# Performance work log

Hardware: AMD Instinct MI355X
Metric: run time of the kernel (lower is better)

## Reference

```python
import jax, jax.numpy as jnp
import numpy as np

B, S, D, E, K = 4, 4096, 2048, 64, 2
LN_EPS = 1e-5
TEMP_EPS = 1e-6
Z_LOSS_COEF = 0.001
LB_COEF = 0.1


def setup_inputs() -> dict:
    key = jax.random.key(0)
    k1, k2 = jax.random.split(key)
    x = jax.random.normal(k1, (B, S, D), dtype=jnp.float32)
    # kaiming_normal fan_in (std = 1/sqrt(D)) scaled by 0.01, as in __init__
    W = jax.random.normal(k2, (E, D), dtype=jnp.float32) * jnp.float32(0.01 / np.sqrt(D))
    gamma = jnp.ones((E,), jnp.float32)   # LayerNorm weight
    beta = jnp.zeros((E,), jnp.float32)   # LayerNorm bias
    temperature = jnp.full((1,), 0.5, jnp.float32)
    return {"x": x, "W": W, "gamma": gamma, "beta": beta, "temperature": temperature}


def reference(x, W, gamma, beta, temperature):
    b, s, d = x.shape
    xf = x.reshape(-1, d)                                  # [N, D]
    logits = xf @ W.T                                      # [N, E]
    # LayerNorm over expert dim (biased variance, eps=1e-5, matches torch)
    mu = logits.mean(axis=-1, keepdims=True)
    var = jnp.mean(jnp.square(logits - mu), axis=-1, keepdims=True)
    logits = (logits - mu) * jax.lax.rsqrt(var + LN_EPS) * gamma + beta
    # temperature-scaled softmax
    routing_weights = jax.nn.softmax(logits / (temperature + TEMP_EPS), axis=-1)  # [N, E]
    # top-k + scatter into dense dispatch mask
    top_w, top_idx = jax.lax.top_k(routing_weights, K)     # [N, K]
    n = routing_weights.shape[0]
    dispatch = jnp.zeros_like(routing_weights).at[jnp.arange(n)[:, None], top_idx].set(top_w)
    dispatch = dispatch.reshape(b, s, E)                   # [B, S, E]
    # aux losses
    expert_load = dispatch.mean(axis=1)                    # [B, E]
    load_balance_loss = jnp.std(expert_load, ddof=1) / expert_load.mean() * 10.0
    router_z_loss = jnp.mean(jnp.square(logits))
    total_loss = ZLC * router_z_loss + LB_COEF * load_balance_loss if False else (
        Z_LOSS_COEF * router_z_loss + LB_COEF * load_balance_loss)
    return jax.lax.stop_gradient(routing_weights), dispatch, total_loss
```

## Files before the change

kernel.cpp:

```cpp
#include <hip/hip_runtime.h>
#include <hip/hip_bf16.h>
#include <float.h>
#include <math.h>

#define B_DIM 4
#define S_DIM 4096
#define D_DIM 2048
#define E_DIM 64
#define N_TOK 16384
#define SPLITK 4
#define KSLICE (D_DIM / SPLITK)
#define MSTEP (KSLICE / 32)
#define TPB 128
#define NMAIN ((N_TOK / TPB) * SPLITK)
#define EPB 16
#define NEPI (N_TOK / EPB)
#define GAP_THRESH 1e-3f

#define WS_WLO_B   262144
#define WS_HEAD_B  524288
#define WS_PART_B  540672
#define WS_NEED    (WS_PART_B + (size_t)SPLITK * N_TOK * E_DIM * 4)
#define HEAD_ZSLOT 0
#define HEAD_LOADP 64

typedef __bf16 bf16x8_t __attribute__((ext_vector_type(8)));
typedef float f32x4_t __attribute__((ext_vector_type(4)));
union U8 { bf16x8_t v; unsigned short u[8]; };

__device__ __forceinline__ void split2(float f, unsigned short& h, unsigned short& l) {
    unsigned int u = __float_as_uint(f);
    h = (unsigned short)(u >> 16);
    float hf = __uint_as_float(u & 0xFFFF0000u);
    l = (unsigned short)(__float_as_uint(f - hf) >> 16);
}

__global__ __launch_bounds__(256) void wconv(const float* __restrict__ W,
                                             unsigned short* __restrict__ whi,
                                             unsigned short* __restrict__ wlo) {
    const int t = blockIdx.x * 256 + threadIdx.x;
    float4 v = *(const float4*)(W + (size_t)t * 4);
    ushort4 h, l;
    split2(v.x, h.x, l.x); split2(v.y, h.y, l.y);
    split2(v.z, h.z, l.z); split2(v.w, h.w, l.w);
    *(ushort4*)(whi + (size_t)t * 4) = h;
    *(ushort4*)(wlo + (size_t)t * 4) = l;
}

template<bool ATOMIC>
__global__ __launch_bounds__(256, 2) void router_main(
    const float* __restrict__ x,
    const unsigned short* __restrict__ whi, const unsigned short* __restrict__ wlo,
    float* __restrict__ part)
{
    const int tid = threadIdx.x;
    const int lane = tid & 63, wv = tid >> 6;
    const int l15 = lane & 15, quad = lane >> 4;
    const int slice = blockIdx.x & (SPLITK - 1);
    const int grp = blockIdx.x >> 2;
    const int tokBase = grp * TPB + wv * 32;
    const int k0 = slice * KSLICE;

    const float* xb[2];
    xb[0] = x + (size_t)(tokBase + l15) * D_DIM + k0 + quad * 8;
    xb[1] = x + (size_t)(tokBase + 16 + l15) * D_DIM + k0 + quad * 8;

    f32x4_t acc[2][4];
    #pragma unroll
    for (int m = 0; m < 2; ++m)
        #pragma unroll
        for (int t = 0; t < 4; ++t) acc[m][t] = (f32x4_t){0.f, 0.f, 0.f, 0.f};

    float4 xq[2][2], xn[2][2];
    #pragma unroll
    for (int m = 0; m < 2; ++m) {
        xq[m][0] = *(const float4*)(xb[m]);
        xq[m][1] = *(const float4*)(xb[m] + 4);
    }

    #pragma unroll 4
    for (int s = 0; s < MSTEP; ++s) {
        if (s + 1 < MSTEP) {
            #pragma unroll
            for (int m = 0; m < 2; ++m) {
                const float* p = xb[m] + (s + 1) * 32;
                xn[m][0] = *(const float4*)(p);
                xn[m][1] = *(const float4*)(p + 4);
            }
        }
        const int kk = k0 + s * 32 + quad * 8;
        bf16x8_t bh[4], bl[4];
        #pragma unroll
        for (int t = 0; t < 4; ++t) {
            const size_t off = (size_t)(t * 16 + l15) * D_DIM + kk;
            bh[t] = *(const bf16x8_t*)(whi + off);
            bl[t] = *(const bf16x8_t*)(wlo + off);
        }
        #pragma unroll
        for (int m = 0; m < 2; ++m) {
            float tf[8] = {xq[m][0].x, xq[m][0].y, xq[m][0].z, xq[m][0].w,
                           xq[m][1].x, xq[m][1].y, xq[m][1].z, xq[m][1].w};
            U8 ah, al;
            #pragma unroll
            for (int k = 0; k < 8; ++k) split2(tf[k], ah.u[k], al.u[k]);
            #pragma unroll
            for (int t = 0; t < 4; ++t) {
                acc[m][t] = __builtin_amdgcn_mfma_f32_16x16x32_bf16(ah.v, bh[t], acc[m][t], 0, 0, 0);
                acc[m][t] = __builtin_amdgcn_mfma_f32_16x16x32_bf16(ah.v, bl[t], acc[m][t], 0, 0, 0);
                acc[m][t] = __builtin_amdgcn_mfma_f32_16x16x32_bf16(al.v, bh[t], acc[m][t], 0, 0, 0);
            }
        }
        if (s + 1 < MSTEP) {
            #pragma unroll
            for (int m = 0; m < 2; ++m) { xq[m][0] = xn[m][0]; xq[m][1] = xn[m][1]; }
        }
    }

    #pragma unroll
    for (int m = 0; m < 2; ++m)
        #pragma unroll
        for (int t = 0; t < 4; ++t)
            #pragma unroll
            for (int r = 0; r < 4; ++r) {
                const int token = tokBase + m * 16 + quad * 4 + r;
                const int e = t * 16 + l15;
                if (ATOMIC) atomicAdd(&part[(size_t)token * E_DIM + e], acc[m][t][r]);
                else part[((size_t)slice * N_TOK + token) * E_DIM + e] = acc[m][t][r];
            }
}

__device__ __forceinline__ void wave_argmax(float y, float& mv, int& mi) {
    float v = y; int ix = threadIdx.x & 63;
    #pragma unroll
    for (int d = 32; d; d >>= 1) {
        float ov = __shfl_xor(v, d); int oi = __shfl_xor(ix, d);
        if (ov > v || (ov == v && oi < ix)) { v = ov; ix = oi; }
    }
    mv = v; mi = ix;
}

template<bool ATOMIC>
__global__ __launch_bounds__(1024) void router_epi(
    const float* __restrict__ part, const float* __restrict__ x,
    const float* __restrict__ W, const float* __restrict__ gamma,
    const float* __restrict__ beta, const float* __restrict__ temperature,
    float* __restrict__ out_rw, float* __restrict__ out_dp,
    float* __restrict__ zslot, float* __restrict__ loadp)
{
    __shared__ float loadsum[E_DIM];
    __shared__ float zred[EPB];
    const int tid = threadIdx.x;
    const int lane = tid & 63, wv = tid >> 6;
    const int tok = blockIdx.x * EPB + wv;
    if (tid < E_DIM) loadsum[tid] = 0.f;
    __syncthreads();

    float p;
    if (ATOMIC) p = part[(size_t)tok * E_DIM + lane];
    else {
        p = 0.f;
        #pragma unroll
        for (int s = 0; s < SPLITK; ++s) p += part[((size_t)s * N_TOK + tok) * E_DIM + lane];
    }
    float s1 = p, s2 = p * p;
    #pragma unroll
    for (int d = 32; d; d >>= 1) { s1 += __shfl_xor(s1, d); s2 += __shfl_xor(s2, d); }
    const float mu = s1 * (1.f / 64.f);
    const float var = s2 * (1.f / 64.f) - mu * mu;
    const float rs = rsqrtf(var + 1e-5f);
    const float y = (p - mu) * rs * gamma[lane] + beta[lane];

    float zl = y * y;
    #pragma unroll
    for (int d = 32; d; d >>= 1) zl += __shfl_xor(zl, d);
    if (lane == 0) zred[wv] = zl;

    float m0, m1, m2; int i0, i1, i2;
    wave_argmax(y, m0, i0);
    wave_argmax((lane == i0) ? -FLT_MAX : y, m1, i1);
    wave_argmax((lane == i0 || lane == i1) ? -FLT_MAX : y, m2, i2);
    int sa = i0, sb = i1;

    if (m1 - m2 < GAP_THRESH) {
        const float* xr = x + (size_t)tok * D_DIM;
        const int c[3] = {i0, i1, i2};
        double L[3];
        #pragma unroll
        for (int j = 0; j < 3; ++j) {
            const float* wr = W + (size_t)c[j] * D_DIM;
            double a = 0.0;
            for (int i = lane; i < D_DIM; i += 64) a += (double)xr[i] * (double)wr[i];
            #pragma unroll
            for (int d = 32; d; d >>= 1) a += __shfl_xor(a, d);
            L[j] = a;
        }
        double yy[3];
        #pragma unroll
        for (int j = 0; j < 3; ++j)
            yy[j] = (L[j] - (double)mu) * (double)rs * (double)gamma[c[j]] + (double)beta[c[j]];
        bool g01 = (yy[0] > yy[1]) || (yy[0] == yy[1] && c[0] < c[1]);
        bool g02 = (yy[0] > yy[2]) || (yy[0] == yy[2] && c[0] < c[2]);
        bool g12 = (yy[1] > yy[2]) || (yy[1] == yy[2] && c[1] < c[2]);
        if (!g01 && !g02)     { sa = c[1]; sb = c[2]; }
        else if (g01 && !g12) { sa = c[0]; sb = c[2]; }
        else                  { sa = c[0]; sb = c[1]; }
    }

    const float it = 1.f / (temperature[0] + 1e-6f);
    float ev = __expf((y - m0) * it);
    float es = ev;
    #pragma unroll
    for (int d = 32; d; d >>= 1) es += __shfl_xor(es, d);
    const float prob = ev / es;

    out_rw[(size_t)tok * E_DIM + lane] = prob;
    const bool sel = (lane == sa || lane == sb);
    out_dp[(size_t)tok * E_DIM + lane] = sel ? prob : 0.f;
    if (sel) atomicAdd(&loadsum[lane], prob);
    __syncthreads();

    if (tid == 0) {
        float z = 0.f;
        #pragma unroll
        for (int i = 0; i < EPB; ++i) z += zred[i];
        atomicAdd(&zslot[blockIdx.x & 63], z);
    }
    const int b = (blockIdx.x * EPB) >> 12;
    if (tid < E_DIM) atomicAdd(&loadp[(blockIdx.x & 7) * 256 + b * E_DIM + tid], loadsum[tid]);
}

__global__ void router_fin(const float* __restrict__ head, float* __restrict__ out_loss) {
    __shared__ float sv[B_DIM * E_DIM];
    const int tid = threadIdx.x;
    float s = 0.f;
    #pragma unroll
    for (int pl = 0; pl < 8; ++pl) s += head[HEAD_LOADP + pl * 256 + tid];
    sv[tid] = s * (1.f / S_DIM);
    __syncthreads();
    if (tid == 0) {
        float t = 0.f;
        for (int i = 0; i < B_DIM * E_DIM; ++i) t += sv[i];
        const float mean = t * (1.f / (B_DIM * E_DIM));
        float ss = 0.f;
        for (int i = 0; i < B_DIM * E_DIM; ++i) { float d = sv[i] - mean; ss += d * d; }
        const float sd = sqrtf(ss * (1.f / (B_DIM * E_DIM - 1)));
        float z = 0.f;
        for (int i = 0; i < 64; ++i) z += head[HEAD_ZSLOT + i];
        out_loss[0] = 0.001f * (z * (1.f / ((float)N_TOK * E_DIM))) + 0.1f * (sd / mean) * 10.f;
    }
}

extern "C" void kernel_launch(void* const* d_in, const int* in_sizes, int n_in,
                              void* d_out, int out_size, void* d_ws, size_t ws_size,
                              hipStream_t stream) {
    const float* x     = (const float*)d_in[0];
    const float* W     = (const float*)d_in[1];
    const float* gamma = (const float*)d_in[2];
    const float* beta  = (const float*)d_in[3];
    const float* temp  = (const float*)d_in[4];
    float* out  = (float*)d_out;
    float* rw   = out;
    float* dp   = out + (size_t)N_TOK * E_DIM;
    float* loss = out + 2 * (size_t)N_TOK * E_DIM;

    unsigned short* whi = (unsigned short*)d_ws;
    unsigned short* wlo = (unsigned short*)((char*)d_ws + WS_WLO_B);
    float* head = (float*)((char*)d_ws + WS_HEAD_B);
    float* partbuf = (float*)((char*)d_ws + WS_PART_B);
    const bool store_path = (ws_size >= WS_NEED);

    hipMemsetAsync((char*)d_ws + WS_HEAD_B, 0, 16384, stream);
    wconv<<<dim3(128), dim3(256), 0, stream>>>(W, whi, wlo);
    if (store_path) {
        router_main<false><<<dim3(NMAIN), dim3(256), 0, stream>>>(x, whi, wlo, partbuf);
        router_epi<false><<<dim3(NEPI), dim3(1024), 0, stream>>>(
            partbuf, x, W, gamma, beta, temp, rw, dp,
            head + HEAD_ZSLOT, head + HEAD_LOADP);
    } else {
        hipMemsetAsync(rw, 0, (size_t)N_TOK * E_DIM * 4, stream);
        router_main<true><<<dim3(NMAIN), dim3(256), 0, stream>>>(x, whi, wlo, rw);
        router_epi<true><<<dim3(NEPI), dim3(1024), 0, stream>>>(
            rw, x, W, gamma, beta, temp, rw, dp,
            head + HEAD_ZSLOT, head + HEAD_LOADP);
    }
    router_fin<<<dim3(1), dim3(256), 0, stream>>>(head, loss);
}
```

Before: 270.5 us.

## Use single bf16 MFMA with LDS-staged weights and widen exact top-k fallback

Replaces the three-pass split-bf16 GEMM with a single bf16 MFMA pass using round-to-nearest conversion. Each block now stages its W slice as bf16 in LDS, which removes the separate weight-conversion kernel. To absorb the larger logit error, the gap threshold for the fp64 recheck is raised and the candidate set grows from three to four experts. The epilogue drops its LDS reductions in favour of direct per-lane global atomics, so more tokens may take the slow fp64 path and contention on the atomics goes up.

```diff
diff --git a/kernel.cpp b/kernel.cpp
--- a/kernel.cpp
+++ b/kernel.cpp
@@ -10,123 +10,88 @@
 #define N_TOK 16384
 #define SPLITK 4
 #define KSLICE (D_DIM / SPLITK)
-#define MSTEP (KSLICE / 32)
-#define TPB 128
-#define NMAIN ((N_TOK / TPB) * SPLITK)
-#define EPB 16
-#define NEPI (N_TOK / EPB)
-#define GAP_THRESH 1e-3f
-
-#define WS_WLO_B   262144
-#define WS_HEAD_B  524288
-#define WS_PART_B  540672
-#define WS_NEED    (WS_PART_B + (size_t)SPLITK * N_TOK * E_DIM * 4)
+#define STEPS (KSLICE / 32)
+#define TPB_MAIN 256
+#define NMAIN ((N_TOK / TPB_MAIN) * SPLITK)
+#define NEPI (N_TOK / 4)
+#define PITCH 520
+#define GAP_THRESH 0.02f
+
 #define HEAD_ZSLOT 0
 #define HEAD_LOADP 64
+#define WS_PART_B  16384
+#define WS_NEED    (WS_PART_B + (size_t)SPLITK * N_TOK * E_DIM * 4)
 
 typedef __bf16 bf16x8_t __attribute__((ext_vector_type(8)));
 typedef float f32x4_t __attribute__((ext_vector_type(4)));
 union U8 { bf16x8_t v; unsigned short u[8]; };
 
-__device__ __forceinline__ void split2(float f, unsigned short& h, unsigned short& l) {
+__device__ __forceinline__ unsigned short f2bf(float f) {
     unsigned int u = __float_as_uint(f);
-    h = (unsigned short)(u >> 16);
-    float hf = __uint_as_float(u & 0xFFFF0000u);
-    l = (unsigned short)(__float_as_uint(f - hf) >> 16);
-}
-
-__global__ __launch_bounds__(256) void wconv(const float* __restrict__ W,
-                                             unsigned short* __restrict__ whi,
-                                             unsigned short* __restrict__ wlo) {
-    const int t = blockIdx.x * 256 + threadIdx.x;
-    float4 v = *(const float4*)(W + (size_t)t * 4);
-    ushort4 h, l;
-    split2(v.x, h.x, l.x); split2(v.y, h.y, l.y);
-    split2(v.z, h.z, l.z); split2(v.w, h.w, l.w);
-    *(ushort4*)(whi + (size_t)t * 4) = h;
-    *(ushort4*)(wlo + (size_t)t * 4) = l;
+    u += 0x7FFFu + ((u >> 16) & 1u);
+    return (unsigned short)(u >> 16);
 }
 
 template<bool ATOMIC>
-__global__ __launch_bounds__(256, 2) void router_main(
-    const float* __restrict__ x,
-    const unsigned short* __restrict__ whi, const unsigned short* __restrict__ wlo,
+__global__ __launch_bounds__(1024, 4) void router_main(
+    const float* __restrict__ x, const float* __restrict__ W,
     float* __restrict__ part)
 {
+    __shared__ unsigned short wlds[E_DIM][PITCH];
     const int tid = threadIdx.x;
+    const int slice = blockIdx.x & (SPLITK - 1);
+    const int grp = blockIdx.x >> 2;
+
+    {
+        const int row = tid >> 4, seg = tid & 15;
+        const float* wp = W + (size_t)row * D_DIM + slice * KSLICE + seg * 32;
+        #pragma unroll
+        for (int j = 0; j < 8; ++j) {
+            float4 v = *(const float4*)(wp + j * 4);
+            ushort4 h = {f2bf(v.x), f2bf(v.y), f2bf(v.z), f2bf(v.w)};
+            *(ushort4*)&wlds[row][seg * 32 + j * 4] = h;
+        }
+    }
+    __syncthreads();
+
     const int lane = tid & 63, wv = tid >> 6;
     const int l15 = lane & 15, quad = lane >> 4;
-    const int slice = blockIdx.x & (SPLITK - 1);
-    const int grp = blockIdx.x >> 2;
-    const int tokBase = grp * TPB + wv * 32;
-    const int k0 = slice * KSLICE;
-
-    const float* xb[2];
-    xb[0] = x + (size_t)(tokBase + l15) * D_DIM + k0 + quad * 8;
-    xb[1] = x + (size_t)(tokBase + 16 + l15) * D_DIM + k0 + quad * 8;
-
-    f32x4_t acc[2][4];
-    #pragma unroll
-    for (int m = 0; m < 2; ++m)
-        #pragma unroll
-        for (int t = 0; t < 4; ++t) acc[m][t] = (f32x4_t){0.f, 0.f, 0.f, 0.f};
-
-    float4 xq[2][2], xn[2][2];
-    #pragma unroll
-    for (int m = 0; m < 2; ++m) {
-        xq[m][0] = *(const float4*)(xb[m]);
-        xq[m][1] = *(const float4*)(xb[m] + 4);
-    }
-
+    const int token0 = grp * TPB_MAIN + wv * 16;
+    const float* xp = x + (size_t)(token0 + l15) * D_DIM + slice * KSLICE + quad * 8;
+
+    f32x4_t acc[4];
+    #pragma unroll
+    for (int t = 0; t < 4; ++t) acc[t] = (f32x4_t){0.f, 0.f, 0.f, 0.f};
+
+    float4 xq0 = *(const float4*)xp;
+    float4 xq1 = *(const float4*)(xp + 4);
     #pragma unroll 4
-    for (int s = 0; s < MSTEP; ++s) {
-        if (s + 1 < MSTEP) {
-            #pragma unroll
-            for (int m = 0; m < 2; ++m) {
-                const float* p = xb[m] + (s + 1) * 32;
-                xn[m][0] = *(const float4*)(p);
-                xn[m][1] = *(const float4*)(p + 4);
-            }
-        }
-        const int kk = k0 + s * 32 + quad * 8;
-        bf16x8_t bh[4], bl[4];
+    for (int s = 0; s < STEPS; ++s) {
+        float4 xn0, xn1;
+        if (s + 1 < STEPS) {
+            xn0 = *(const float4*)(xp + (s + 1) * 32);
+            xn1 = *(const float4*)(xp + (s + 1) * 32 + 4);
+        }
+        U8 a;
+        a.u[0] = f2bf(xq0.x); a.u[1] = f2bf(xq0.y); a.u[2] = f2bf(xq0.z); a.u[3] = f2bf(xq0.w);
+        a.u[4] = f2bf(xq1.x); a.u[5] = f2bf(xq1.y); a.u[6] = f2bf(xq1.z); a.u[7] = f2bf(xq1.w);
         #pragma unroll
         for (int t = 0; t < 4; ++t) {
-            const size_t off = (size_t)(t * 16 + l15) * D_DIM + kk;
-            bh[t] = *(const bf16x8_t*)(whi + off);
-            bl[t] = *(const bf16x8_t*)(wlo + off);
-        }
-        #pragma unroll
-        for (int m = 0; m < 2; ++m) {
-            float tf[8] = {xq[m][0].x, xq[m][0].y, xq[m][0].z, xq[m][0].w,
-                           xq[m][1].x, xq[m][1].y, xq[m][1].z, xq[m][1].w};
-            U8 ah, al;
-            #pragma unroll
-            for (int k = 0; k < 8; ++k) split2(tf[k], ah.u[k], al.u[k]);
-            #pragma unroll
-            for (int t = 0; t < 4; ++t) {
-                acc[m][t] = __builtin_amdgcn_mfma_f32_16x16x32_bf16(ah.v, bh[t], acc[m][t], 0, 0, 0);
-                acc[m][t] = __builtin_amdgcn_mfma_f32_16x16x32_bf16(ah.v, bl[t], acc[m][t], 0, 0, 0);
-                acc[m][t] = __builtin_amdgcn_mfma_f32_16x16x32_bf16(al.v, bh[t], acc[m][t], 0, 0, 0);
-            }
-        }
-        if (s + 1 < MSTEP) {
-            #pragma unroll
-            for (int m = 0; m < 2; ++m) { xq[m][0] = xn[m][0]; xq[m][1] = xn[m][1]; }
-        }
-    }
-
-    #pragma unroll
-    for (int m = 0; m < 2; ++m)
-        #pragma unroll
-        for (int t = 0; t < 4; ++t)
-            #pragma unroll
-            for (int r = 0; r < 4; ++r) {
-                const int token = tokBase + m * 16 + quad * 4 + r;
-                const int e = t * 16 + l15;
-                if (ATOMIC) atomicAdd(&part[(size_t)token * E_DIM + e], acc[m][t][r]);
-                else part[((size_t)slice * N_TOK + token) * E_DIM + e] = acc[m][t][r];
-            }
+            bf16x8_t b = *(const bf16x8_t*)&wlds[t * 16 + l15][s * 32 + quad * 8];
+            acc[t] = __builtin_amdgcn_mfma_f32_16x16x32_bf16(a.v, b, acc[t], 0, 0, 0);
+        }
+        if (s + 1 < STEPS) { xq0 = xn0; xq1 = xn1; }
+    }
+
+    #pragma unroll
+    for (int t = 0; t < 4; ++t)
+        #pragma unroll
+        for (int r = 0; r < 4; ++r) {
+            const int token = token0 + quad * 4 + r;
+            const int e = t * 16 + l15;
+            if (ATOMIC) atomicAdd(&part[(size_t)token * E_DIM + e], acc[t][r]);
+            else part[((size_t)slice * N_TOK + token) * E_DIM + e] = acc[t][r];
+        }
 }
 
 __device__ __forceinline__ void wave_argmax(float y, float& mv, int& mi) {
@@ -140,20 +105,16 @@
 }
 
 template<bool ATOMIC>
-__global__ __launch_bounds__(1024) void router_epi(
+__global__ __launch_bounds__(256, 4) void router_epi(
     const float* __restrict__ part, const float* __restrict__ x,
     const float* __restrict__ W, const float* __restrict__ gamma,
     const float* __restrict__ beta, const float* __restrict__ temperature,
     float* __restrict__ out_rw, float* __restrict__ out_dp,
     float* __restrict__ zslot, float* __restrict__ loadp)
 {
-    __shared__ float loadsum[E_DIM];
-    __shared__ float zred[EPB];
     const int tid = threadIdx.x;
     const int lane = tid & 63, wv = tid >> 6;
-    const int tok = blockIdx.x * EPB + wv;
-    if (tid < E_DIM) loadsum[tid] = 0.f;
-    __syncthreads();
+    const int tok = blockIdx.x * 4 + wv;
 
     float p;
     if (ATOMIC) p = part[(size_t)tok * E_DIM + lane];
@@ -173,37 +134,36 @@
     float zl = y * y;
     #pragma unroll
     for (int d = 32; d; d >>= 1) zl += __shfl_xor(zl, d);
-    if (lane == 0) zred[wv] = zl;
-
-    float m0, m1, m2; int i0, i1, i2;
+
+    float m0, m1, m2, m3; int i0, i1, i2, i3;
     wave_argmax(y, m0, i0);
     wave_argmax((lane == i0) ? -FLT_MAX : y, m1, i1);
     wave_argmax((lane == i0 || lane == i1) ? -FLT_MAX : y, m2, i2);
+    wave_argmax((lane == i0 || lane == i1 || lane == i2) ? -FLT_MAX : y, m3, i3);
     int sa = i0, sb = i1;
 
     if (m1 - m2 < GAP_THRESH) {
         const float* xr = x + (size_t)tok * D_DIM;
-        const int c[3] = {i0, i1, i2};
-        double L[3];
-        #pragma unroll
-        for (int j = 0; j < 3; ++j) {
-            const float* wr = W + (size_t)c[j] * D_DIM;
+        const int cc[4] = {i0, i1, i2, i3};
+        double yy[4];
+        #pragma unroll
+        for (int j = 0; j < 4; ++j) {
+            const float* wr = W + (size_t)cc[j] * D_DIM;
             double a = 0.0;
             for (int i = lane; i < D_DIM; i += 64) a += (double)xr[i] * (double)wr[i];
             #pragma unroll
             for (int d = 32; d; d >>= 1) a += __shfl_xor(a, d);
-            L[j] = a;
-        }
-        double yy[3];
-        #pragma unroll
-        for (int j = 0; j < 3; ++j)
-            yy[j] = (L[j] - (double)mu) * (double)rs * (double)gamma[c[j]] + (double)beta[c[j]];
-        bool g01 = (yy[0] > yy[1]) || (yy[0] == yy[1] && c[0] < c[1]);
-        bool g02 = (yy[0] > yy[2]) || (yy[0] == yy[2] && c[0] < c[2]);
-        bool g12 = (yy[1] > yy[2]) || (yy[1] == yy[2] && c[1] < c[2]);
-        if (!g01 && !g02)     { sa = c[1]; sb = c[2]; }
-        else if (g01 && !g12) { sa = c[0]; sb = c[2]; }
-        else                  { sa = c[0]; sb = c[1]; }
+            yy[j] = (a - (double)mu) * (double)rs * (double)gamma[cc[j]] + (double)beta[cc[j]];
+        }
+        int a4 = 0;
+        #pragma unroll
+        for (int j = 1; j < 4; ++j)
+            if (yy[j] > yy[a4] || (yy[j] == yy[a4] && cc[j] < cc[a4])) a4 = j;
+        int b4 = (a4 == 0) ? 1 : 0;
+        #pragma unroll
+        for (int j = 0; j < 4; ++j)
+            if (j != a4 && (yy[j] > yy[b4] || (yy[j] == yy[b4] && cc[j] < cc[b4]))) b4 = j;
+        sa = cc[a4]; sb = cc[b4];
     }
 
     const float it = 1.f / (temperature[0] + 1e-6f);
@@ -216,17 +176,8 @@
     out_rw[(size_t)tok * E_DIM + lane] = prob;
     const bool sel = (lane == sa || lane == sb);
     out_dp[(size_t)tok * E_DIM + lane] = sel ? prob : 0.f;
-    if (sel) atomicAdd(&loadsum[lane], prob);
-    __syncthreads();
-
-    if (tid == 0) {
-        float z = 0.f;
-        #pragma unroll
-        for (int i = 0; i < EPB; ++i) z += zred[i];
-        atomicAdd(&zslot[blockIdx.x & 63], z);
-    }
-    const int b = (blockIdx.x * EPB) >> 12;
-    if (tid < E_DIM) atomicAdd(&loadp[(blockIdx.x & 7) * 256 + b * E_DIM + tid], loadsum[tid]);
+    if (sel) atomicAdd(&loadp[(blockIdx.x & 7) * 256 + (tok >> 12) * E_DIM + lane], prob);
+    if (lane == 0) atomicAdd(&zslot[blockIdx.x & 63], zl);
 }
 
 __global__ void router_fin(const float* __restrict__ head, float* __restrict__ out_loss) {
@@ -263,23 +214,20 @@
     float* dp   = out + (size_t)N_TOK * E_DIM;
     float* loss = out + 2 * (size_t)N_TOK * E_DIM;
 
-    unsigned short* whi = (unsigned short*)d_ws;
-    unsigned short* wlo = (unsigned short*)((char*)d_ws + WS_WLO_B);
-    float* head = (float*)((char*)d_ws + WS_HEAD_B);
+    float* head = (float*)d_ws;
     float* partbuf = (float*)((char*)d_ws + WS_PART_B);
     const bool store_path = (ws_size >= WS_NEED);
 
-    hipMemsetAsync((char*)d_ws + WS_HEAD_B, 0, 16384, stream);
-    wconv<<<dim3(128), dim3(256), 0, stream>>>(W, whi, wlo);
+    hipMemsetAsync(d_ws, 0, WS_PART_B, stream);
     if (store_path) {
-        router_main<false><<<dim3(NMAIN), dim3(256), 0, stream>>>(x, whi, wlo, partbuf);
-        router_epi<false><<<dim3(NEPI), dim3(1024), 0, stream>>>(
+        router_main<false><<<dim3(NMAIN), dim3(1024), 0, stream>>>(x, W, partbuf);
+        router_epi<false><<<dim3(NEPI), dim3(256), 0, stream>>>(
             partbuf, x, W, gamma, beta, temp, rw, dp,
             head + HEAD_ZSLOT, head + HEAD_LOADP);
     } else {
         hipMemsetAsync(rw, 0, (size_t)N_TOK * E_DIM * 4, stream);
-        router_main<true><<<dim3(NMAIN), dim3(256), 0, stream>>>(x, whi, wlo, rw);
-        router_epi<true><<<dim3(NEPI), dim3(1024), 0, stream>>>(
+        router_main<true><<<dim3(NMAIN), dim3(1024), 0, stream>>>(x, W, rw);
+        router_epi<true><<<dim3(NEPI), dim3(256), 0, stream>>>(
             rw, x, W, gamma, beta, temp, rw, dp,
             head + HEAD_ZSLOT, head + HEAD_LOADP);
     }
```

After: 337.0 us. +24.6%, slower.
